# Performance work log

Hardware: AMD Instinct MI355X
Metric: run time of the kernel (lower is better)

## Reference

```python
import jax, jax.numpy as jnp
import numpy as np


def setup_inputs() -> dict:
    key = jax.random.key(0)
    k1, k2, k3 = jax.random.split(key, 3)
    B, H, L, OUT = 4096, 2048, 8, 1024
    x = jax.random.normal(k1, (B, H), dtype=jnp.float32)
    W = jax.random.normal(k2, (L, H, H), dtype=jnp.float32)
    beta = jax.random.normal(k3, (H, OUT), dtype=jnp.float32)
    return {"x": x, "W": W, "beta": beta}


def _fcn_forward(x, W, beta):
    h = W.shape[-1]
    scale = 1.0 / jnp.sqrt(jnp.asarray(h, x.dtype))
    # Linear1d: (x[:,None]*W).sum(-1)/sqrt(h) == x @ W.T / sqrt(h); then ReLU.
    def layer(y, Wi):
        y = jax.nn.relu(jnp.einsum('bi,oi->bo', y, Wi) * scale)
        return y, None
    y, _ = jax.lax.scan(layer, x, W)
    # readout: y @ beta / h
    return jnp.einsum('bh,ho->bo', y, beta) / h


def reference(x, W, beta):
    return _fcn_forward(x, W, beta)
```

## Files before the change

### kernel.cpp

```cpp
#include <hip/hip_runtime.h>
#include <cstdint>
#include <cstddef>

typedef __bf16          bf16x8  __attribute__((ext_vector_type(8)));
typedef float           f32x4   __attribute__((ext_vector_type(4)));
typedef unsigned short  u16x8   __attribute__((ext_vector_type(8)));

__device__ __forceinline__ unsigned short f32_bf16_rne(float f) {
  union { float f; unsigned u; } v; v.f = f;
  unsigned u = v.u + 0x7FFFu + ((v.u >> 16) & 1u);
  return (unsigned short)(u >> 16);
}

__global__ void cvt_f32_bf16(const float* __restrict__ in,
                             unsigned short* __restrict__ out, int n8) {
  int idx = blockIdx.x * 256 + threadIdx.x;
  int stride = gridDim.x * 256;
  for (int i = idx; i < n8; i += stride) {
    float4 a = ((const float4*)in)[2 * (size_t)i];
    float4 b = ((const float4*)in)[2 * (size_t)i + 1];
    u16x8 o;
    o[0] = f32_bf16_rne(a.x); o[1] = f32_bf16_rne(a.y);
    o[2] = f32_bf16_rne(a.z); o[3] = f32_bf16_rne(a.w);
    o[4] = f32_bf16_rne(b.x); o[5] = f32_bf16_rne(b.y);
    o[6] = f32_bf16_rne(b.z); o[7] = f32_bf16_rne(b.w);
    *(u16x8*)(out + (size_t)i * 8) = o;
  }
}

__global__ void cvt_transpose(const float* __restrict__ in,
                              unsigned short* __restrict__ out, int H, int O) {
  __shared__ float tile[32][33];
  int o0 = blockIdx.x * 32, h0 = blockIdx.y * 32;
  int tx = threadIdx.x & 31, ty = threadIdx.x >> 5;
  #pragma unroll
  for (int i = ty; i < 32; i += 8)
    tile[i][tx] = in[(size_t)(h0 + i) * O + (o0 + tx)];
  __syncthreads();
  #pragma unroll
  for (int i = ty; i < 32; i += 8)
    out[(size_t)(o0 + i) * H + (h0 + tx)] = f32_bf16_rne(tile[tx][i]);
}

#define GLOAD(gp, lp)                                                   \
  __builtin_amdgcn_global_load_lds(                                     \
      (const __attribute__((address_space(1))) void*)(gp),              \
      (__attribute__((address_space(3))) void*)(lp), 16, 0, 0)

#define MFMA16 __builtin_amdgcn_mfma_f32_16x16x32_bf16

__device__ __forceinline__ void read_frags(bf16x8 (&fa)[2][4], bf16x8 (&fb)[2][4],
                                           const __bf16* sa, const __bf16* sb,
                                           int aBase, int bBase, int cc0, int cc1) {
  #pragma unroll
  for (int kk = 0; kk < 2; ++kk) {
    const int c = kk ? cc1 : cc0;
    #pragma unroll
    for (int m = 0; m < 4; ++m)
      fa[kk][m] = *(const bf16x8*)(sa + aBase + m * 1024 + c);
    #pragma unroll
    for (int n = 0; n < 4; ++n)
      fb[kk][n] = *(const bf16x8*)(sb + bBase + n * 1024 + c);
  }
}

__device__ __forceinline__ void mfma32(f32x4 (&acc)[4][4],
                                       const bf16x8 (&fa)[2][4],
                                       const bf16x8 (&fb)[2][4]) {
  #pragma unroll
  for (int kk = 0; kk < 2; ++kk)
    #pragma unroll
    for (int m = 0; m < 4; ++m)
      #pragma unroll
      for (int n = 0; n < 4; ++n)
        acc[m][n] = MFMA16(fa[kk][m], fb[kk][n], acc[m][n], 0, 0, 0);
}


#define BODY(T, FA_C, FB_C, FA_N, FB_N)                                   \
  do {                                                                    \
    const int t_ = (T);                                                   \
    if (t_ + 2 < NT) {                                                    \
      const size_t ko = (size_t)(t_ + 2) * 64;                            \
      __bf16* dA = As + sst * 8192;                                       \
      __bf16* dB = Bs + sst * 16384;                                      \
      GLOAD(gA0 + ko, dA + 0 * 4096 + tid * 8);                           \
      GLOAD(gA1 + ko, dA + 1 * 4096 + tid * 8);                           \
      GLOAD(gB0 + ko, dB + 0 * 4096 + tid * 8);                           \
      GLOAD(gB1 + ko, dB + 1 * 4096 + tid * 8);                           \
      GLOAD(gB2 + ko, dB + 2 * 4096 + tid * 8);                           \
      GLOAD(gB3 + ko, dB + 3 * 4096 + tid * 8);                           \
      asm volatile("s_waitcnt lgkmcnt(0)" ::: "memory");                  \
      asm volatile("s_waitcnt vmcnt(6)" ::: "memory");                    \
    } else {                                                              \
      asm volatile("s_waitcnt lgkmcnt(0)" ::: "memory");                  \
      asm volatile("s_waitcnt vmcnt(0)" ::: "memory");                    \
    }                                                                     \
    __builtin_amdgcn_s_barrier();                                         \
    __builtin_amdgcn_sched_barrier(0);                                    \
    if (t_ + 1 < NT)                                                      \
      read_frags(FA_N, FB_N, As + srd * 8192, Bs + srd * 16384,           \
                 aBase, bBase, cc0, cc1);                                 \
    __builtin_amdgcn_s_setprio(1);                                        \
    mfma32(acc, FA_C, FB_C);                                              \
    __builtin_amdgcn_s_setprio(0);                                        \
    sst = sst + 1; if (sst == 3) sst = 0;                                 \
    srd = srd + 1; if (srd == 3) srd = 0;                                 \
  } while (0)

__global__ __launch_bounds__(512, 2)
void gemm128x256p(const unsigned short* __restrict__ A,
                  const unsigned short* __restrict__ B,
                  unsigned short* __restrict__ Cp, int N, int K, float scale) {
  __shared__ __bf16 As[3 * 128 * 64] __attribute__((aligned(16)));
  __shared__ __bf16 Bs[3 * 256 * 64] __attribute__((aligned(16)));

  const int tid  = threadIdx.x;
  const int lane = tid & 63;
  const int wave = tid >> 6;
  const int wr   = wave >> 2;
  const int wc   = wave & 3;
  const int l16  = lane & 15;
  const int kgrp = lane >> 4;

  const int brow0 = blockIdx.y * 128;
  const int bcol0 = blockIdx.x * 256;

  const int xorv  = (l16 & 7) << 3;
  const int cc0   = (kgrp * 8) ^ xorv;
  const int cc1   = (32 + kgrp * 8) ^ xorv;
  const int aBase = (wr * 64 + l16) * 64;
  const int bBase = (wc * 64 + l16) * 64;

  const int srow = tid >> 3;
  const int scol = ((tid & 7) * 8) ^ ((srow & 7) << 3);
  const unsigned short* gA0 = A + (size_t)(brow0 +   0 + srow) * K + scol;
  const unsigned short* gA1 = A + (size_t)(brow0 +  64 + srow) * K + scol;
  const unsigned short* gB0 = B + (size_t)(bcol0 +   0 + srow) * K + scol;
  const unsigned short* gB1 = B + (size_t)(bcol0 +  64 + srow) * K + scol;
  const unsigned short* gB2 = B + (size_t)(bcol0 + 128 + srow) * K + scol;
  const unsigned short* gB3 = B + (size_t)(bcol0 + 192 + srow) * K + scol;

  f32x4  acc[4][4] = {};
  bf16x8 fa0[2][4], fb0[2][4], fa1[2][4], fb1[2][4];

  const int NT = K >> 6;

  {
    GLOAD(gA0, &As[0 * 4096 + tid * 8]);
    GLOAD(gA1, &As[1 * 4096 + tid * 8]);
    GLOAD(gB0, &Bs[0 * 4096 + tid * 8]);
    GLOAD(gB1, &Bs[1 * 4096 + tid * 8]);
    GLOAD(gB2, &Bs[2 * 4096 + tid * 8]);
    GLOAD(gB3, &Bs[3 * 4096 + tid * 8]);
    GLOAD(gA0 + 64, &As[8192 + 0 * 4096 + tid * 8]);
    GLOAD(gA1 + 64, &As[8192 + 1 * 4096 + tid * 8]);
    GLOAD(gB0 + 64, &Bs[16384 + 0 * 4096 + tid * 8]);
    GLOAD(gB1 + 64, &Bs[16384 + 1 * 4096 + tid * 8]);
    GLOAD(gB2 + 64, &Bs[16384 + 2 * 4096 + tid * 8]);
    GLOAD(gB3 + 64, &Bs[16384 + 3 * 4096 + tid * 8]);
    asm volatile("s_waitcnt vmcnt(6)" ::: "memory");
    __builtin_amdgcn_s_barrier();
    read_frags(fa0, fb0, As, Bs, aBase, bBase, cc0, cc1);
  }

  int sst = 2, srd = 1;
  for (int t = 0; t < NT; t += 2) {
    BODY(t,     fa0, fb0, fa1, fb1);
    BODY(t + 1, fa1, fb1, fa0, fb0);
  }

  const int crow0 = brow0 + wr * 64 + kgrp * 4;
  const int ccol0 = bcol0 + wc * 64 + l16;
  #pragma unroll
  for (int m = 0; m < 4; ++m)
    #pragma unroll
    for (int n = 0; n < 4; ++n)
      #pragma unroll
      for (int j = 0; j < 4; ++j) {
        float v = acc[m][n][j] * scale;
        v = v > 0.0f ? v : 0.0f;
        Cp[(size_t)(crow0 + m * 16 + j) * N + (ccol0 + n * 16)] = f32_bf16_rne(v);
      }
}

__global__ __launch_bounds__(256)
void gemm_bt_f32(const unsigned short* __restrict__ A,
                 const unsigned short* __restrict__ B,
                 float* __restrict__ C, int N, int K, float scale) {
  __shared__ __bf16 As[128 * 32] __attribute__((aligned(16)));
  __shared__ __bf16 Bs[128 * 32] __attribute__((aligned(16)));

  const int tid  = threadIdx.x;
  const int lane = tid & 63;
  const int wave = tid >> 6;
  const int wr   = wave >> 1, wc = wave & 1;
  const int l16  = lane & 15, kgrp = lane >> 4;

  const int brow0 = blockIdx.y * 128;
  const int bcol0 = blockIdx.x * 128;

  const int offb  = wave * 2048 + lane * 16;
  const int srow  = offb >> 6;
  const int selem = (offb & 63) >> 1;
  const unsigned short* gA0 = A + (size_t)(brow0 + srow) * K + selem;
  const unsigned short* gA1 = A + (size_t)(brow0 + srow + 16) * K + selem;
  const unsigned short* gB0 = B + (size_t)(bcol0 + srow) * K + selem;
  const unsigned short* gB1 = B + (size_t)(bcol0 + srow + 16) * K + selem;
  __bf16* lA0 = &As[wave * 1024];
  __bf16* lA1 = &As[wave * 1024 + 512];
  __bf16* lB0 = &Bs[wave * 1024];
  __bf16* lB1 = &Bs[wave * 1024 + 512];

  f32x4 acc[4][4] = {};
  const int aoff = (wr * 64 + l16) * 32 + kgrp * 8;
  const int boff = (wc * 64 + l16) * 32 + kgrp * 8;

  for (int k0 = 0; k0 < K; k0 += 32) {
    GLOAD(gA0 + k0, lA0);
    GLOAD(gA1 + k0, lA1);
    GLOAD(gB0 + k0, lB0);
    GLOAD(gB1 + k0, lB1);
    asm volatile("s_waitcnt vmcnt(0)" ::: "memory");
    __syncthreads();

    bf16x8 af[4], bfv[4];
    #pragma unroll
    for (int m = 0; m < 4; ++m)
      af[m] = *(const bf16x8*)(As + aoff + m * 16 * 32);
    #pragma unroll
    for (int n = 0; n < 4; ++n)
      bfv[n] = *(const bf16x8*)(Bs + boff + n * 16 * 32);
    #pragma unroll
    for (int m = 0; m < 4; ++m)
      #pragma unroll
      for (int n = 0; n < 4; ++n)
        acc[m][n] = MFMA16(af[m], bfv[n], acc[m][n], 0, 0, 0);
    __syncthreads();
  }

  const int crow0 = brow0 + wr * 64 + kgrp * 4;
  const int ccol0 = bcol0 + wc * 64 + l16;
  #pragma unroll
  for (int m = 0; m < 4; ++m)
    #pragma unroll
    for (int n = 0; n < 4; ++n)
      #pragma unroll
      for (int j = 0; j < 4; ++j)
        C[(size_t)(crow0 + m * 16 + j) * N + (ccol0 + n * 16)] =
            acc[m][n][j] * scale;
}

extern "C" void kernel_launch(void* const* d_in, const int* in_sizes, int n_in,
                              void* d_out, int out_size, void* d_ws, size_t ws_size,
                              hipStream_t stream) {
  const float* x    = (const float*)d_in[0];
  const float* W    = (const float*)d_in[1];
  const float* beta = (const float*)d_in[2];
  float* out = (float*)d_out;

  const int Bn = 4096, H = 2048, L = 8, O = 1024;

  unsigned short* y0    = (unsigned short*)d_ws;
  unsigned short* y1    = y0 + (size_t)Bn * H;
  unsigned short* Wb    = y1 + (size_t)Bn * H;
  unsigned short* betaT = Wb + (size_t)L * H * H;

  {
    int n8 = L * H * H / 8;
    cvt_f32_bf16<<<2048, 256, 0, stream>>>(W, Wb, n8);
  }
  {
    int n8 = Bn * H / 8;
    int grid = (n8 + 255) / 256;
    if (grid > 2048) grid = 2048;
    cvt_f32_bf16<<<grid, 256, 0, stream>>>(x, y0, n8);
  }
  cvt_transpose<<<dim3(O / 32, H / 32), 256, 0, stream>>>(beta, betaT, H, O);

  const float s1 = 0.02209708691207961f;
  unsigned short* yin = y0;
  unsigned short* yout = y1;
  for (int l = 0; l < L; ++l) {
    gemm128x256p<<<dim3(H / 256, Bn / 128), 512, 0, stream>>>(
        yin, Wb + (size_t)l * H * H, yout, H, H, s1);
    unsigned short* t = yin; yin = yout; yout = t;
  }
  gemm_bt_f32<<<dim3(O / 128, Bn / 128), 256, 0, stream>>>(yin, betaT, out, O, H,
                                                           1.0f / 2048.0f);
}
```

Baseline: 404.6 us.

## Rework layer GEMM to 4 waves with 128x64 per-wave tiles and 3-stage prefetch

The hidden-layer GEMM moves from 8 waves of 64x64 tiles to 4 waves that each compute the full 128 rows by 64 columns, doubling per-wave accumulators and MFMA work per LDS fragment load. The prefetch depth grows from two stages to three in flight. Explicit sched_group_barrier interleaving mixes MFMAs with DS reads and global-to-LDS loads, and the final tiles are drained by a peeled epilogue. This aims to cut LDS traffic per FLOP and hide global latency better, at the cost of higher register pressure and only one block per CU, which lowers occupancy.

```diff
diff --git a/kernel.cpp b/kernel.cpp
--- a/kernel.cpp
+++ b/kernel.cpp
@@ -49,67 +49,86 @@
 
 #define MFMA16 __builtin_amdgcn_mfma_f32_16x16x32_bf16
 
-__device__ __forceinline__ void read_frags(bf16x8 (&fa)[2][4], bf16x8 (&fb)[2][4],
-                                           const __bf16* sa, const __bf16* sb,
-                                           int aBase, int bBase, int cc0, int cc1) {
+
+__device__ __forceinline__ void read_frags24(bf16x8 (&fa)[2][8], bf16x8 (&fb)[2][4],
+                                             const __bf16* sa, const __bf16* sb,
+                                             int l16, int bBase, int cc0, int cc1) {
   #pragma unroll
   for (int kk = 0; kk < 2; ++kk) {
     const int c = kk ? cc1 : cc0;
     #pragma unroll
-    for (int m = 0; m < 4; ++m)
-      fa[kk][m] = *(const bf16x8*)(sa + aBase + m * 1024 + c);
+    for (int m = 0; m < 8; ++m)
+      fa[kk][m] = *(const bf16x8*)(sa + (m * 16 + l16) * 64 + c);
     #pragma unroll
     for (int n = 0; n < 4; ++n)
       fb[kk][n] = *(const bf16x8*)(sb + bBase + n * 1024 + c);
   }
 }
 
-__device__ __forceinline__ void mfma32(f32x4 (&acc)[4][4],
-                                       const bf16x8 (&fa)[2][4],
+__device__ __forceinline__ void mfma64(f32x4 (&acc)[8][4],
+                                       const bf16x8 (&fa)[2][8],
                                        const bf16x8 (&fb)[2][4]) {
   #pragma unroll
   for (int kk = 0; kk < 2; ++kk)
     #pragma unroll
-    for (int m = 0; m < 4; ++m)
+    for (int m = 0; m < 8; ++m)
       #pragma unroll
       for (int n = 0; n < 4; ++n)
         acc[m][n] = MFMA16(fa[kk][m], fb[kk][n], acc[m][n], 0, 0, 0);
 }
 
-
-#define BODY(T, FA_C, FB_C, FA_N, FB_N)                                   \
+#define STAGE12(KO, DA, DB)                                               \
   do {                                                                    \
-    const int t_ = (T);                                                   \
-    if (t_ + 2 < NT) {                                                    \
-      const size_t ko = (size_t)(t_ + 2) * 64;                            \
+    GLOAD(gA0 + (KO), (DA) + 0 * 2048 + tid * 8);                         \
+    GLOAD(gA1 + (KO), (DA) + 1 * 2048 + tid * 8);                         \
+    GLOAD(gA2 + (KO), (DA) + 2 * 2048 + tid * 8);                         \
+    GLOAD(gA3 + (KO), (DA) + 3 * 2048 + tid * 8);                         \
+    GLOAD(gB0 + (KO), (DB) + 0 * 2048 + tid * 8);                         \
+    GLOAD(gB1 + (KO), (DB) + 1 * 2048 + tid * 8);                         \
+    GLOAD(gB2 + (KO), (DB) + 2 * 2048 + tid * 8);                         \
+    GLOAD(gB3 + (KO), (DB) + 3 * 2048 + tid * 8);                         \
+    GLOAD(gB4 + (KO), (DB) + 4 * 2048 + tid * 8);                         \
+    GLOAD(gB5 + (KO), (DB) + 5 * 2048 + tid * 8);                         \
+    GLOAD(gB6 + (KO), (DB) + 6 * 2048 + tid * 8);                         \
+    GLOAD(gB7 + (KO), (DB) + 7 * 2048 + tid * 8);                         \
+  } while (0)
+
+#define SGB_INTERLEAVE                                                    \
+  do {                                                                    \
+    _Pragma("unroll")                                                     \
+    for (int g_ = 0; g_ < 8; ++g_) {                                      \
+      __builtin_amdgcn_sched_group_barrier(0x008, 8, 0);     \
+      __builtin_amdgcn_sched_group_barrier(0x100, 3, 0);     \
+      if (g_ < 6)                                                         \
+        __builtin_amdgcn_sched_group_barrier(0x010, 2, 0);    \
+    }                                                                     \
+  } while (0)
+
+#define BODY_R(T, FAC, FBC, FAN, FBN)                                     \
+  do {                                                                    \
+    asm volatile("s_waitcnt vmcnt(12)" ::: "memory");                     \
+    asm volatile("s_waitcnt lgkmcnt(0)" ::: "memory");                    \
+    __builtin_amdgcn_s_barrier();                                         \
+    __builtin_amdgcn_sched_barrier(0);                                    \
+    {                                                                     \
+      const size_t ko = (size_t)((T) + 3) * 64;                           \
       __bf16* dA = As + sst * 8192;                                       \
       __bf16* dB = Bs + sst * 16384;                                      \
-      GLOAD(gA0 + ko, dA + 0 * 4096 + tid * 8);                           \
-      GLOAD(gA1 + ko, dA + 1 * 4096 + tid * 8);                           \
-      GLOAD(gB0 + ko, dB + 0 * 4096 + tid * 8);                           \
-      GLOAD(gB1 + ko, dB + 1 * 4096 + tid * 8);                           \
-      GLOAD(gB2 + ko, dB + 2 * 4096 + tid * 8);                           \
-      GLOAD(gB3 + ko, dB + 3 * 4096 + tid * 8);                           \
-      asm volatile("s_waitcnt lgkmcnt(0)" ::: "memory");                  \
-      asm volatile("s_waitcnt vmcnt(6)" ::: "memory");                    \
-    } else {                                                              \
-      asm volatile("s_waitcnt lgkmcnt(0)" ::: "memory");                  \
-      asm volatile("s_waitcnt vmcnt(0)" ::: "memory");                    \
+      STAGE12(ko, dA, dB);                                                \
+      read_frags24(FAN, FBN, As + srd * 8192, Bs + srd * 16384,           \
+                   l16, bBase, cc0, cc1);                                 \
+      __builtin_amdgcn_s_setprio(1);                                      \
+      mfma64(acc, FAC, FBC);                                              \
+      __builtin_amdgcn_s_setprio(0);                                      \
+      SGB_INTERLEAVE;                                                     \
+      __builtin_amdgcn_sched_barrier(0);                                  \
     }                                                                     \
-    __builtin_amdgcn_s_barrier();                                         \
-    __builtin_amdgcn_sched_barrier(0);                                    \
-    if (t_ + 1 < NT)                                                      \
-      read_frags(FA_N, FB_N, As + srd * 8192, Bs + srd * 16384,           \
-                 aBase, bBase, cc0, cc1);                                 \
-    __builtin_amdgcn_s_setprio(1);                                        \
-    mfma32(acc, FA_C, FB_C);                                              \
-    __builtin_amdgcn_s_setprio(0);                                        \
-    sst = sst + 1; if (sst == 3) sst = 0;                                 \
-    srd = srd + 1; if (srd == 3) srd = 0;                                 \
+    sst = sst + 1 == 3 ? 0 : sst + 1;                                     \
+    srd = srd + 1 == 3 ? 0 : srd + 1;                                     \
   } while (0)
 
-__global__ __launch_bounds__(512, 2)
-void gemm128x256p(const unsigned short* __restrict__ A,
+__global__ __launch_bounds__(256, 1)
+void gemm128x256w(const unsigned short* __restrict__ A,
                   const unsigned short* __restrict__ B,
                   unsigned short* __restrict__ Cp, int N, int K, float scale) {
   __shared__ __bf16 As[3 * 128 * 64] __attribute__((aligned(16)));
@@ -118,8 +137,6 @@
   const int tid  = threadIdx.x;
   const int lane = tid & 63;
   const int wave = tid >> 6;
-  const int wr   = wave >> 2;
-  const int wc   = wave & 3;
   const int l16  = lane & 15;
   const int kgrp = lane >> 4;
 
@@ -129,51 +146,80 @@
   const int xorv  = (l16 & 7) << 3;
   const int cc0   = (kgrp * 8) ^ xorv;
   const int cc1   = (32 + kgrp * 8) ^ xorv;
-  const int aBase = (wr * 64 + l16) * 64;
-  const int bBase = (wc * 64 + l16) * 64;
+  const int bBase = (wave * 64 + l16) * 64;
 
   const int srow = tid >> 3;
   const int scol = ((tid & 7) * 8) ^ ((srow & 7) << 3);
   const unsigned short* gA0 = A + (size_t)(brow0 +   0 + srow) * K + scol;
-  const unsigned short* gA1 = A + (size_t)(brow0 +  64 + srow) * K + scol;
+  const unsigned short* gA1 = A + (size_t)(brow0 +  32 + srow) * K + scol;
+  const unsigned short* gA2 = A + (size_t)(brow0 +  64 + srow) * K + scol;
+  const unsigned short* gA3 = A + (size_t)(brow0 +  96 + srow) * K + scol;
   const unsigned short* gB0 = B + (size_t)(bcol0 +   0 + srow) * K + scol;
-  const unsigned short* gB1 = B + (size_t)(bcol0 +  64 + srow) * K + scol;
-  const unsigned short* gB2 = B + (size_t)(bcol0 + 128 + srow) * K + scol;
-  const unsigned short* gB3 = B + (size_t)(bcol0 + 192 + srow) * K + scol;
-
-  f32x4  acc[4][4] = {};
-  bf16x8 fa0[2][4], fb0[2][4], fa1[2][4], fb1[2][4];
+  const unsigned short* gB1 = B + (size_t)(bcol0 +  32 + srow) * K + scol;
+  const unsigned short* gB2 = B + (size_t)(bcol0 +  64 + srow) * K + scol;
+  const unsigned short* gB3 = B + (size_t)(bcol0 +  96 + srow) * K + scol;
+  const unsigned short* gB4 = B + (size_t)(bcol0 + 128 + srow) * K + scol;
+  const unsigned short* gB5 = B + (size_t)(bcol0 + 160 + srow) * K + scol;
+  const unsigned short* gB6 = B + (size_t)(bcol0 + 192 + srow) * K + scol;
+  const unsigned short* gB7 = B + (size_t)(bcol0 + 224 + srow) * K + scol;
+
+  f32x4  acc[8][4] = {};
+  bf16x8 fa0[2][8], fb0[2][4], fa1[2][8], fb1[2][4];
 
   const int NT = K >> 6;
 
   {
-    GLOAD(gA0, &As[0 * 4096 + tid * 8]);
-    GLOAD(gA1, &As[1 * 4096 + tid * 8]);
-    GLOAD(gB0, &Bs[0 * 4096 + tid * 8]);
-    GLOAD(gB1, &Bs[1 * 4096 + tid * 8]);
-    GLOAD(gB2, &Bs[2 * 4096 + tid * 8]);
-    GLOAD(gB3, &Bs[3 * 4096 + tid * 8]);
-    GLOAD(gA0 + 64, &As[8192 + 0 * 4096 + tid * 8]);
-    GLOAD(gA1 + 64, &As[8192 + 1 * 4096 + tid * 8]);
-    GLOAD(gB0 + 64, &Bs[16384 + 0 * 4096 + tid * 8]);
-    GLOAD(gB1 + 64, &Bs[16384 + 1 * 4096 + tid * 8]);
-    GLOAD(gB2 + 64, &Bs[16384 + 2 * 4096 + tid * 8]);
-    GLOAD(gB3 + 64, &Bs[16384 + 3 * 4096 + tid * 8]);
-    asm volatile("s_waitcnt vmcnt(6)" ::: "memory");
+    STAGE12((size_t)0,   As + 0 * 8192, Bs + 0 * 16384);
+    STAGE12((size_t)64,  As + 1 * 8192, Bs + 1 * 16384);
+    STAGE12((size_t)128, As + 2 * 8192, Bs + 2 * 16384);
+    asm volatile("s_waitcnt vmcnt(24)" ::: "memory");
     __builtin_amdgcn_s_barrier();
-    read_frags(fa0, fb0, As, Bs, aBase, bBase, cc0, cc1);
-  }
-
-  int sst = 2, srd = 1;
-  for (int t = 0; t < NT; t += 2) {
-    BODY(t,     fa0, fb0, fa1, fb1);
-    BODY(t + 1, fa1, fb1, fa0, fb0);
-  }
-
-  const int crow0 = brow0 + wr * 64 + kgrp * 4;
-  const int ccol0 = bcol0 + wc * 64 + l16;
-  #pragma unroll
-  for (int m = 0; m < 4; ++m)
+    read_frags24(fa0, fb0, As, Bs, l16, bBase, cc0, cc1);
+  }
+
+  int sst = 0, srd = 1;
+  for (int t = 0; t < NT - 4; t += 2) {
+    BODY_R(t,     fa0, fb0, fa1, fb1);
+    BODY_R(t + 1, fa1, fb1, fa0, fb0);
+  }
+  BODY_R(NT - 4, fa0, fb0, fa1, fb1);
+
+  {
+    asm volatile("s_waitcnt vmcnt(12)" ::: "memory");
+    asm volatile("s_waitcnt lgkmcnt(0)" ::: "memory");
+    __builtin_amdgcn_s_barrier();
+    __builtin_amdgcn_sched_barrier(0);
+    read_frags24(fa0, fb0, As + srd * 8192, Bs + srd * 16384,
+                 l16, bBase, cc0, cc1);
+    __builtin_amdgcn_s_setprio(1);
+    mfma64(acc, fa1, fb1);
+    __builtin_amdgcn_s_setprio(0);
+    __builtin_amdgcn_sched_barrier(0);
+    srd = srd + 1 == 3 ? 0 : srd + 1;
+  }
+  {
+    asm volatile("s_waitcnt vmcnt(0)" ::: "memory");
+    asm volatile("s_waitcnt lgkmcnt(0)" ::: "memory");
+    __builtin_amdgcn_s_barrier();
+    __builtin_amdgcn_sched_barrier(0);
+    read_frags24(fa1, fb1, As + srd * 8192, Bs + srd * 16384,
+                 l16, bBase, cc0, cc1);
+    __builtin_amdgcn_s_setprio(1);
+    mfma64(acc, fa0, fb0);
+    __builtin_amdgcn_s_setprio(0);
+    __builtin_amdgcn_sched_barrier(0);
+  }
+  {
+    asm volatile("s_waitcnt lgkmcnt(0)" ::: "memory");
+    __builtin_amdgcn_s_setprio(1);
+    mfma64(acc, fa1, fb1);
+    __builtin_amdgcn_s_setprio(0);
+  }
+
+  const int crow0 = brow0 + kgrp * 4;
+  const int ccol0 = bcol0 + wave * 64 + l16;
+  #pragma unroll
+  for (int m = 0; m < 8; ++m)
     #pragma unroll
     for (int n = 0; n < 4; ++n)
       #pragma unroll
@@ -282,7 +328,7 @@
   unsigned short* yin = y0;
   unsigned short* yout = y1;
   for (int l = 0; l < L; ++l) {
-    gemm128x256p<<<dim3(H / 256, Bn / 128), 512, 0, stream>>>(
+    gemm128x256w<<<dim3(H / 256, Bn / 128), 256, 0, stream>>>(
         yin, Wb + (size_t)l * H * H, yout, H, H, s1);
     unsigned short* t = yin; yin = yout; yout = t;
   }
```

New measurement: 612.0 us. 51.3% more time.

## Load B fragments directly from global into registers, stage only A in LDS

Applied to the files above, without the earlier changes.

The layer GEMM now stops staging the W (B) tile in LDS. Each wave loads its B MFMA fragments straight from global memory into registers one k-step ahead. A is still shared through a double-buffered LDS tile, but it is now staged via register loads and ds_writes instead of global_load_lds with a triple buffer. This cuts LDS footprint and LDS read traffic for B, and may allow higher occupancy. The cost is uncoalesced 16-byte global reads of B, duplicated across the two wave rows, and more registers holding prefetched fragments.

```diff
diff --git a/kernel.cpp b/kernel.cpp
--- a/kernel.cpp
+++ b/kernel.cpp
@@ -49,21 +49,6 @@
 
 #define MFMA16 __builtin_amdgcn_mfma_f32_16x16x32_bf16
 
-__device__ __forceinline__ void read_frags(bf16x8 (&fa)[2][4], bf16x8 (&fb)[2][4],
-                                           const __bf16* sa, const __bf16* sb,
-                                           int aBase, int bBase, int cc0, int cc1) {
-  #pragma unroll
-  for (int kk = 0; kk < 2; ++kk) {
-    const int c = kk ? cc1 : cc0;
-    #pragma unroll
-    for (int m = 0; m < 4; ++m)
-      fa[kk][m] = *(const bf16x8*)(sa + aBase + m * 1024 + c);
-    #pragma unroll
-    for (int n = 0; n < 4; ++n)
-      fb[kk][n] = *(const bf16x8*)(sb + bBase + n * 1024 + c);
-  }
-}
-
 __device__ __forceinline__ void mfma32(f32x4 (&acc)[4][4],
                                        const bf16x8 (&fa)[2][4],
                                        const bf16x8 (&fb)[2][4]) {
@@ -77,43 +62,49 @@
 }
 
 
-#define BODY(T, FA_C, FB_C, FA_N, FB_N)                                   \
+#define BODYR(T, SCUR, SNXT, BCUR, BNXT, AR0, AR1, AW0, AW1)              \
   do {                                                                    \
     const int t_ = (T);                                                   \
+    bf16x8 fa[2][4];                                                      \
+    {                                                                     \
+      const __bf16* rA = As + (SCUR) * 8192;                              \
+      _Pragma("unroll")                                                   \
+      for (int m = 0; m < 4; ++m) {                                       \
+        fa[0][m] = *(const bf16x8*)(rA + (aRow + m * 16) * 64 + cc0);     \
+        fa[1][m] = *(const bf16x8*)(rA + (aRow + m * 16) * 64 + cc1);     \
+      }                                                                   \
+    }                                                                     \
+    if (t_ + 1 < NT) {                                                    \
+      const size_t bko = (size_t)(t_ + 1) * 64;                           \
+      _Pragma("unroll")                                                   \
+      for (int n = 0; n < 4; ++n) {                                       \
+        BNXT[0][n] = *(const bf16x8*)(gB + n * bstride + bko);            \
+        BNXT[1][n] = *(const bf16x8*)(gB + n * bstride + bko + 32);       \
+      }                                                                   \
+    }                                                                     \
     if (t_ + 2 < NT) {                                                    \
-      const size_t ko = (size_t)(t_ + 2) * 64;                            \
-      __bf16* dA = As + sst * 8192;                                       \
-      __bf16* dB = Bs + sst * 16384;                                      \
-      GLOAD(gA0 + ko, dA + 0 * 4096 + tid * 8);                           \
-      GLOAD(gA1 + ko, dA + 1 * 4096 + tid * 8);                           \
-      GLOAD(gB0 + ko, dB + 0 * 4096 + tid * 8);                           \
-      GLOAD(gB1 + ko, dB + 1 * 4096 + tid * 8);                           \
-      GLOAD(gB2 + ko, dB + 2 * 4096 + tid * 8);                           \
-      GLOAD(gB3 + ko, dB + 3 * 4096 + tid * 8);                           \
-      asm volatile("s_waitcnt lgkmcnt(0)" ::: "memory");                  \
-      asm volatile("s_waitcnt vmcnt(6)" ::: "memory");                    \
-    } else {                                                              \
-      asm volatile("s_waitcnt lgkmcnt(0)" ::: "memory");                  \
-      asm volatile("s_waitcnt vmcnt(0)" ::: "memory");                    \
-    }                                                                     \
+      const size_t ako = (size_t)(t_ + 2) * 64;                           \
+      AR0 = *(const bf16x8*)(gA0 + ako);                                  \
+      AR1 = *(const bf16x8*)(gA1 + ako);                                  \
+    }                                                                     \
+    __builtin_amdgcn_s_setprio(1);                                        \
+    mfma32(acc, fa, BCUR);                                                \
+    __builtin_amdgcn_s_setprio(0);                                        \
+    if (t_ + 1 < NT) {                                                    \
+      __bf16* wA = As + (SNXT) * 8192;                                    \
+      *(bf16x8*)(wA + wOff0) = AW0;                                       \
+      *(bf16x8*)(wA + wOff1) = AW1;                                       \
+    }                                                                     \
+    asm volatile("s_waitcnt lgkmcnt(0)" ::: "memory");                    \
     __builtin_amdgcn_s_barrier();                                         \
     __builtin_amdgcn_sched_barrier(0);                                    \
-    if (t_ + 1 < NT)                                                      \
-      read_frags(FA_N, FB_N, As + srd * 8192, Bs + srd * 16384,           \
-                 aBase, bBase, cc0, cc1);                                 \
-    __builtin_amdgcn_s_setprio(1);                                        \
-    mfma32(acc, FA_C, FB_C);                                              \
-    __builtin_amdgcn_s_setprio(0);                                        \
-    sst = sst + 1; if (sst == 3) sst = 0;                                 \
-    srd = srd + 1; if (srd == 3) srd = 0;                                 \
   } while (0)
 
 __global__ __launch_bounds__(512, 2)
-void gemm128x256p(const unsigned short* __restrict__ A,
+void gemm128x256r(const unsigned short* __restrict__ A,
                   const unsigned short* __restrict__ B,
                   unsigned short* __restrict__ Cp, int N, int K, float scale) {
-  __shared__ __bf16 As[3 * 128 * 64] __attribute__((aligned(16)));
-  __shared__ __bf16 Bs[3 * 256 * 64] __attribute__((aligned(16)));
+  __shared__ __bf16 As[2 * 128 * 64] __attribute__((aligned(16)));
 
   const int tid  = threadIdx.x;
   const int lane = tid & 63;
@@ -126,48 +117,48 @@
   const int brow0 = blockIdx.y * 128;
   const int bcol0 = blockIdx.x * 256;
 
-  const int xorv  = (l16 & 7) << 3;
-  const int cc0   = (kgrp * 8) ^ xorv;
-  const int cc1   = (32 + kgrp * 8) ^ xorv;
-  const int aBase = (wr * 64 + l16) * 64;
-  const int bBase = (wc * 64 + l16) * 64;
-
-  const int srow = tid >> 3;
-  const int scol = ((tid & 7) * 8) ^ ((srow & 7) << 3);
-  const unsigned short* gA0 = A + (size_t)(brow0 +   0 + srow) * K + scol;
-  const unsigned short* gA1 = A + (size_t)(brow0 +  64 + srow) * K + scol;
-  const unsigned short* gB0 = B + (size_t)(bcol0 +   0 + srow) * K + scol;
-  const unsigned short* gB1 = B + (size_t)(bcol0 +  64 + srow) * K + scol;
-  const unsigned short* gB2 = B + (size_t)(bcol0 + 128 + srow) * K + scol;
-  const unsigned short* gB3 = B + (size_t)(bcol0 + 192 + srow) * K + scol;
+  const int xorv = (l16 & 7) << 3;
+  const int cc0  = (kgrp * 8) ^ xorv;
+  const int cc1  = (32 + kgrp * 8) ^ xorv;
+  const int aRow = wr * 64 + l16;
+
+  const int srow  = tid >> 3;
+  const int scolL = (tid & 7) * 8;
+  const int wOff0 = srow * 64 + (scolL ^ ((srow & 7) << 3));
+  const int wOff1 = wOff0 + 64 * 64;
+  const unsigned short* gA0u = A + (size_t)(brow0 +  0 + srow) * K + scolL;
+  const unsigned short* gA1u = A + (size_t)(brow0 + 64 + srow) * K + scolL;
+  const __bf16* gA0 = (const __bf16*)gA0u;
+  const __bf16* gA1 = (const __bf16*)gA1u;
+
+  const __bf16* gB = (const __bf16*)B +
+                     (size_t)(bcol0 + wc * 64 + l16) * K + kgrp * 8;
+  const size_t bstride = (size_t)16 * K;
 
   f32x4  acc[4][4] = {};
-  bf16x8 fa0[2][4], fb0[2][4], fa1[2][4], fb1[2][4];
+  bf16x8 bE[2][4], bO[2][4];
+  bf16x8 aE0, aE1, aO0, aO1;
 
   const int NT = K >> 6;
 
-  {
-    GLOAD(gA0, &As[0 * 4096 + tid * 8]);
-    GLOAD(gA1, &As[1 * 4096 + tid * 8]);
-    GLOAD(gB0, &Bs[0 * 4096 + tid * 8]);
-    GLOAD(gB1, &Bs[1 * 4096 + tid * 8]);
-    GLOAD(gB2, &Bs[2 * 4096 + tid * 8]);
-    GLOAD(gB3, &Bs[3 * 4096 + tid * 8]);
-    GLOAD(gA0 + 64, &As[8192 + 0 * 4096 + tid * 8]);
-    GLOAD(gA1 + 64, &As[8192 + 1 * 4096 + tid * 8]);
-    GLOAD(gB0 + 64, &Bs[16384 + 0 * 4096 + tid * 8]);
-    GLOAD(gB1 + 64, &Bs[16384 + 1 * 4096 + tid * 8]);
-    GLOAD(gB2 + 64, &Bs[16384 + 2 * 4096 + tid * 8]);
-    GLOAD(gB3 + 64, &Bs[16384 + 3 * 4096 + tid * 8]);
-    asm volatile("s_waitcnt vmcnt(6)" ::: "memory");
-    __builtin_amdgcn_s_barrier();
-    read_frags(fa0, fb0, As, Bs, aBase, bBase, cc0, cc1);
-  }
-
-  int sst = 2, srd = 1;
+  aE0 = *(const bf16x8*)(gA0);
+  aE1 = *(const bf16x8*)(gA1);
+  aO0 = *(const bf16x8*)(gA0 + 64);
+  aO1 = *(const bf16x8*)(gA1 + 64);
+  #pragma unroll
+  for (int n = 0; n < 4; ++n) {
+    bE[0][n] = *(const bf16x8*)(gB + n * bstride);
+    bE[1][n] = *(const bf16x8*)(gB + n * bstride + 32);
+  }
+  *(bf16x8*)(As + wOff0) = aE0;
+  *(bf16x8*)(As + wOff1) = aE1;
+  asm volatile("s_waitcnt lgkmcnt(0)" ::: "memory");
+  __builtin_amdgcn_s_barrier();
+  __builtin_amdgcn_sched_barrier(0);
+
   for (int t = 0; t < NT; t += 2) {
-    BODY(t,     fa0, fb0, fa1, fb1);
-    BODY(t + 1, fa1, fb1, fa0, fb0);
+    BODYR(t,     0, 1, bE, bO, aE0, aE1, aO0, aO1);
+    BODYR(t + 1, 1, 0, bO, bE, aO0, aO1, aE0, aE1);
   }
 
   const int crow0 = brow0 + wr * 64 + kgrp * 4;
@@ -282,7 +273,7 @@
   unsigned short* yin = y0;
   unsigned short* yout = y1;
   for (int l = 0; l < L; ++l) {
-    gemm128x256p<<<dim3(H / 256, Bn / 128), 512, 0, stream>>>(
+    gemm128x256r<<<dim3(H / 256, Bn / 128), 512, 0, stream>>>(
         yin, Wb + (size_t)l * H * H, yout, H, H, s1);
     unsigned short* t = yin; yin = yout; yout = t;
   }
```

After: 704.8 us. +74.2%, slower.

## Retile hidden-layer GEMM to 256x128 blocks with 4 waves and BK=32

Applied to the files above, without the earlier changes.

Replaces the 128x256 block tile with 8 waves of 64x64 by a 256x128 tile with 4 waves, each computing a 128x64 sub-tile over a K-step of 32. The goal is more MFMA work per LDS fragment read, since each wave now issues 32 MFMAs per 12 fragment loads instead of 32 per 16. The LDS swizzle and the global-to-LDS load pattern are reworked to match. In exchange each wave holds more accumulators and fragment registers, which may limit occupancy, and the shorter K-step means twice as many barriers per GEMM.

```diff
diff --git a/kernel.cpp b/kernel.cpp
--- a/kernel.cpp
+++ b/kernel.cpp
@@ -49,47 +49,20 @@
 
 #define MFMA16 __builtin_amdgcn_mfma_f32_16x16x32_bf16
 
-__device__ __forceinline__ void read_frags(bf16x8 (&fa)[2][4], bf16x8 (&fb)[2][4],
-                                           const __bf16* sa, const __bf16* sb,
-                                           int aBase, int bBase, int cc0, int cc1) {
-  #pragma unroll
-  for (int kk = 0; kk < 2; ++kk) {
-    const int c = kk ? cc1 : cc0;
-    #pragma unroll
-    for (int m = 0; m < 4; ++m)
-      fa[kk][m] = *(const bf16x8*)(sa + aBase + m * 1024 + c);
-    #pragma unroll
-    for (int n = 0; n < 4; ++n)
-      fb[kk][n] = *(const bf16x8*)(sb + bBase + n * 1024 + c);
-  }
-}
-
-__device__ __forceinline__ void mfma32(f32x4 (&acc)[4][4],
-                                       const bf16x8 (&fa)[2][4],
-                                       const bf16x8 (&fb)[2][4]) {
-  #pragma unroll
-  for (int kk = 0; kk < 2; ++kk)
-    #pragma unroll
-    for (int m = 0; m < 4; ++m)
-      #pragma unroll
-      for (int n = 0; n < 4; ++n)
-        acc[m][n] = MFMA16(fa[kk][m], fb[kk][n], acc[m][n], 0, 0, 0);
-}
-
-
-#define BODY(T, FA_C, FB_C, FA_N, FB_N)                                   \
+
+#define BODY(T, FAC, FBC, FAN, FBN)                                       \
   do {                                                                    \
     const int t_ = (T);                                                   \
     if (t_ + 2 < NT) {                                                    \
-      const size_t ko = (size_t)(t_ + 2) * 64;                            \
+      const size_t ko = (size_t)(t_ + 2) * 32;                            \
       __bf16* dA = As + sst * 8192;                                       \
-      __bf16* dB = Bs + sst * 16384;                                      \
-      GLOAD(gA0 + ko, dA + 0 * 4096 + tid * 8);                           \
-      GLOAD(gA1 + ko, dA + 1 * 4096 + tid * 8);                           \
-      GLOAD(gB0 + ko, dB + 0 * 4096 + tid * 8);                           \
-      GLOAD(gB1 + ko, dB + 1 * 4096 + tid * 8);                           \
-      GLOAD(gB2 + ko, dB + 2 * 4096 + tid * 8);                           \
-      GLOAD(gB3 + ko, dB + 3 * 4096 + tid * 8);                           \
+      __bf16* dB = Bs + sst * 4096;                                       \
+      GLOAD(gA0 + ko, dA + 0 * 2048 + tid * 8);                           \
+      GLOAD(gA1 + ko, dA + 1 * 2048 + tid * 8);                           \
+      GLOAD(gA2 + ko, dA + 2 * 2048 + tid * 8);                           \
+      GLOAD(gA3 + ko, dA + 3 * 2048 + tid * 8);                           \
+      GLOAD(gB0 + ko, dB + 0 * 2048 + tid * 8);                           \
+      GLOAD(gB1 + ko, dB + 1 * 2048 + tid * 8);                           \
       asm volatile("s_waitcnt lgkmcnt(0)" ::: "memory");                  \
       asm volatile("s_waitcnt vmcnt(6)" ::: "memory");                    \
     } else {                                                              \
@@ -98,82 +71,150 @@
     }                                                                     \
     __builtin_amdgcn_s_barrier();                                         \
     __builtin_amdgcn_sched_barrier(0);                                    \
-    if (t_ + 1 < NT)                                                      \
-      read_frags(FA_N, FB_N, As + srd * 8192, Bs + srd * 16384,           \
-                 aBase, bBase, cc0, cc1);                                 \
+    if (t_ + 1 < NT) {                                                    \
+      const __bf16* rA = As + srd * 8192;                                 \
+      const __bf16* rB = Bs + srd * 4096;                                 \
+      _Pragma("unroll")                                                   \
+      for (int m = 0; m < 8; ++m)                                         \
+        FAN[m] = *(const bf16x8*)(rA + (m * 16 + l16) * 32 + cswz);       \
+      _Pragma("unroll")                                                   \
+      for (int n = 0; n < 4; ++n)                                         \
+        FBN[n] = *(const bf16x8*)(rB + (bRow + n * 16) * 32 + cswz);      \
+    }                                                                     \
     __builtin_amdgcn_s_setprio(1);                                        \
-    mfma32(acc, FA_C, FB_C);                                              \
+    _Pragma("unroll")                                                     \
+    for (int m = 0; m < 8; ++m)                                           \
+      _Pragma("unroll")                                                   \
+      for (int n = 0; n < 4; ++n)                                         \
+        acc[m][n] = MFMA16(FAC[m], FBC[n], acc[m][n], 0, 0, 0);           \
     __builtin_amdgcn_s_setprio(0);                                        \
-    sst = sst + 1; if (sst == 3) sst = 0;                                 \
-    srd = srd + 1; if (srd == 3) srd = 0;                                 \
+    sst = sst + 1 == 3 ? 0 : sst + 1;                                     \
+    srd = srd + 1 == 3 ? 0 : srd + 1;                                     \
   } while (0)
 
-__global__ __launch_bounds__(512, 2)
-void gemm128x256p(const unsigned short* __restrict__ A,
+__global__ __launch_bounds__(256, 2)
+void gemm256x128w(const unsigned short* __restrict__ A,
                   const unsigned short* __restrict__ B,
                   unsigned short* __restrict__ Cp, int N, int K, float scale) {
-  __shared__ __bf16 As[3 * 128 * 64] __attribute__((aligned(16)));
-  __shared__ __bf16 Bs[3 * 256 * 64] __attribute__((aligned(16)));
+  __shared__ __bf16 As[3 * 256 * 32] __attribute__((aligned(16)));
+  __shared__ __bf16 Bs[3 * 128 * 32] __attribute__((aligned(16)));
 
   const int tid  = threadIdx.x;
   const int lane = tid & 63;
   const int wave = tid >> 6;
-  const int wr   = wave >> 2;
-  const int wc   = wave & 3;
+  const int wr   = wave >> 1;
+  const int wcN  = wave & 1;
   const int l16  = lane & 15;
   const int kgrp = lane >> 4;
 
-  const int brow0 = blockIdx.y * 128;
-  const int bcol0 = blockIdx.x * 256;
-
-  const int xorv  = (l16 & 7) << 3;
-  const int cc0   = (kgrp * 8) ^ xorv;
-  const int cc1   = (32 + kgrp * 8) ^ xorv;
-  const int aBase = (wr * 64 + l16) * 64;
-  const int bBase = (wc * 64 + l16) * 64;
-
-  const int srow = tid >> 3;
-  const int scol = ((tid & 7) * 8) ^ ((srow & 7) << 3);
+  const int brow0 = blockIdx.y * 256;
+  const int bcol0 = blockIdx.x * 128;
+
+  const int cswz = ((kgrp ^ ((l16 >> 1) & 3)) << 3);
+  const int bRow = wcN * 64;
+  const __bf16* As_wr = nullptr; (void)As_wr;
+
+  const int srow = tid >> 2;
+  const int scol = (((tid & 3) ^ ((srow >> 1) & 3)) << 3);
   const unsigned short* gA0 = A + (size_t)(brow0 +   0 + srow) * K + scol;
   const unsigned short* gA1 = A + (size_t)(brow0 +  64 + srow) * K + scol;
+  const unsigned short* gA2 = A + (size_t)(brow0 + 128 + srow) * K + scol;
+  const unsigned short* gA3 = A + (size_t)(brow0 + 192 + srow) * K + scol;
   const unsigned short* gB0 = B + (size_t)(bcol0 +   0 + srow) * K + scol;
   const unsigned short* gB1 = B + (size_t)(bcol0 +  64 + srow) * K + scol;
-  const unsigned short* gB2 = B + (size_t)(bcol0 + 128 + srow) * K + scol;
-  const unsigned short* gB3 = B + (size_t)(bcol0 + 192 + srow) * K + scol;
-
-  f32x4  acc[4][4] = {};
-  bf16x8 fa0[2][4], fb0[2][4], fa1[2][4], fb1[2][4];
-
-  const int NT = K >> 6;
+
+  f32x4  acc[8][4] = {};
+  bf16x8 fa0[8], fb0[4], fa1[8], fb1[4];
+
+  const int NT = K >> 5;
 
   {
-    GLOAD(gA0, &As[0 * 4096 + tid * 8]);
-    GLOAD(gA1, &As[1 * 4096 + tid * 8]);
-    GLOAD(gB0, &Bs[0 * 4096 + tid * 8]);
-    GLOAD(gB1, &Bs[1 * 4096 + tid * 8]);
-    GLOAD(gB2, &Bs[2 * 4096 + tid * 8]);
-    GLOAD(gB3, &Bs[3 * 4096 + tid * 8]);
-    GLOAD(gA0 + 64, &As[8192 + 0 * 4096 + tid * 8]);
-    GLOAD(gA1 + 64, &As[8192 + 1 * 4096 + tid * 8]);
-    GLOAD(gB0 + 64, &Bs[16384 + 0 * 4096 + tid * 8]);
-    GLOAD(gB1 + 64, &Bs[16384 + 1 * 4096 + tid * 8]);
-    GLOAD(gB2 + 64, &Bs[16384 + 2 * 4096 + tid * 8]);
-    GLOAD(gB3 + 64, &Bs[16384 + 3 * 4096 + tid * 8]);
+    GLOAD(gA0, &As[0 * 2048 + tid * 8]);
+    GLOAD(gA1, &As[1 * 2048 + tid * 8]);
+    GLOAD(gA2, &As[2 * 2048 + tid * 8]);
+    GLOAD(gA3, &As[3 * 2048 + tid * 8]);
+    GLOAD(gB0, &Bs[0 * 2048 + tid * 8]);
+    GLOAD(gB1, &Bs[1 * 2048 + tid * 8]);
+    GLOAD(gA0 + 32, &As[8192 + 0 * 2048 + tid * 8]);
+    GLOAD(gA1 + 32, &As[8192 + 1 * 2048 + tid * 8]);
+    GLOAD(gA2 + 32, &As[8192 + 2 * 2048 + tid * 8]);
+    GLOAD(gA3 + 32, &As[8192 + 3 * 2048 + tid * 8]);
+    GLOAD(gB0 + 32, &Bs[4096 + 0 * 2048 + tid * 8]);
+    GLOAD(gB1 + 32, &Bs[4096 + 1 * 2048 + tid * 8]);
     asm volatile("s_waitcnt vmcnt(6)" ::: "memory");
     __builtin_amdgcn_s_barrier();
-    read_frags(fa0, fb0, As, Bs, aBase, bBase, cc0, cc1);
+    const __bf16* rA = As + (size_t)wr * 0;
+    #pragma unroll
+    for (int m = 0; m < 8; ++m)
+      fa0[m] = *(const bf16x8*)(As + ((wr * 128 + m * 16 + l16) * 32) + cswz);
+    #pragma unroll
+    for (int n = 0; n < 4; ++n)
+      fb0[n] = *(const bf16x8*)(Bs + ((bRow + n * 16 + l16) * 32) + cswz);
+    (void)rA;
   }
 
   int sst = 2, srd = 1;
+  {
+  }
+  const int aWrOff = wr * 128 * 32;
+  #define RDFRAGS(FAN, FBN)                                               \
+    do {                                                                  \
+      const __bf16* rA = As + srd * 8192 + aWrOff;                        \
+      const __bf16* rB = Bs + srd * 4096;                                 \
+      _Pragma("unroll")                                                   \
+      for (int m = 0; m < 8; ++m)                                         \
+        FAN[m] = *(const bf16x8*)(rA + (m * 16 + l16) * 32 + cswz);       \
+      _Pragma("unroll")                                                   \
+      for (int n = 0; n < 4; ++n)                                         \
+        FBN[n] = *(const bf16x8*)(rB + (bRow + n * 16 + l16) * 32 + cswz);\
+    } while (0)
+
+  #define BODY2(T, FAC, FBC, FAN, FBN)                                    \
+    do {                                                                  \
+      const int t_ = (T);                                                 \
+      if (t_ + 2 < NT) {                                                  \
+        const size_t ko = (size_t)(t_ + 2) * 32;                          \
+        __bf16* dA = As + sst * 8192;                                     \
+        __bf16* dB = Bs + sst * 4096;                                     \
+        GLOAD(gA0 + ko, dA + 0 * 2048 + tid * 8);                         \
+        GLOAD(gA1 + ko, dA + 1 * 2048 + tid * 8);                         \
+        GLOAD(gA2 + ko, dA + 2 * 2048 + tid * 8);                         \
+        GLOAD(gA3 + ko, dA + 3 * 2048 + tid * 8);                         \
+        GLOAD(gB0 + ko, dB + 0 * 2048 + tid * 8);                         \
+        GLOAD(gB1 + ko, dB + 1 * 2048 + tid * 8);                         \
+        asm volatile("s_waitcnt lgkmcnt(0)" ::: "memory");                \
+        asm volatile("s_waitcnt vmcnt(6)" ::: "memory");                  \
+      } else {                                                            \
+        asm volatile("s_waitcnt lgkmcnt(0)" ::: "memory");                \
+        asm volatile("s_waitcnt vmcnt(0)" ::: "memory");                  \
+      }                                                                   \
+      __builtin_amdgcn_s_barrier();                                       \
+      __builtin_amdgcn_sched_barrier(0);                                  \
+      if (t_ + 1 < NT) RDFRAGS(FAN, FBN);                                 \
+      __builtin_amdgcn_s_setprio(1);                                      \
+      _Pragma("unroll")                                                   \
+      for (int m = 0; m < 8; ++m)                                         \
+        _Pragma("unroll")                                                 \
+        for (int n = 0; n < 4; ++n)                                       \
+          acc[m][n] = MFMA16(FAC[m], FBC[n], acc[m][n], 0, 0, 0);         \
+      __builtin_amdgcn_s_setprio(0);                                      \
+      sst = sst + 1 == 3 ? 0 : sst + 1;                                   \
+      srd = srd + 1 == 3 ? 0 : srd + 1;                                   \
+    } while (0)
+
+  #pragma unroll
+  for (int m = 0; m < 8; ++m)
+    fa0[m] = *(const bf16x8*)(As + aWrOff + (m * 16 + l16) * 32 + cswz);
+
   for (int t = 0; t < NT; t += 2) {
-    BODY(t,     fa0, fb0, fa1, fb1);
-    BODY(t + 1, fa1, fb1, fa0, fb0);
-  }
-
-  const int crow0 = brow0 + wr * 64 + kgrp * 4;
-  const int ccol0 = bcol0 + wc * 64 + l16;
-  #pragma unroll
-  for (int m = 0; m < 4; ++m)
+    BODY2(t,     fa0, fb0, fa1, fb1);
+    BODY2(t + 1, fa1, fb1, fa0, fb0);
+  }
+
+  const int crow0 = brow0 + wr * 128 + kgrp * 4;
+  const int ccol0 = bcol0 + wcN * 64 + l16;
+  #pragma unroll
+  for (int m = 0; m < 8; ++m)
     #pragma unroll
     for (int n = 0; n < 4; ++n)
       #pragma unroll
@@ -282,7 +323,7 @@
   unsigned short* yin = y0;
   unsigned short* yout = y1;
   for (int l = 0; l < L; ++l) {
-    gemm128x256p<<<dim3(H / 256, Bn / 128), 512, 0, stream>>>(
+    gemm256x128w<<<dim3(H / 128, Bn / 256), 256, 0, stream>>>(
         yin, Wb + (size_t)l * H * H, yout, H, H, s1);
     unsigned short* t = yin; yin = yout; yout = t;
   }
```

Measured after the change: 532.2 us. +31.6%, slower.
